# Kernel tuning notes

Hardware: AMD Instinct MI355X
Metric: run time of the kernel (lower is better)

## Reference

```python
import jax, jax.numpy as jnp
import numpy as np

L = 10
DIL = tuple(2 ** i for i in range(L))  # dilations 1..512, kernel_size=2 -> one past tap, mem_size = dilation
DMAX = max(DIL)
R = 64            # residual channels
G = 2 * R         # gate channels (tanh | sigmoid)
S = 256           # skip channels
MEL = 80
NCLS = 256
HOP = 64
END = 256
FRAMES = 8


def setup_inputs() -> dict:
    ks = jax.random.split(jax.random.key(0), 16)
    sc = jnp.float32(0.1)
    n = lambda k, shape: jax.random.normal(k, shape, jnp.float32) * sc
    return {
        "y": jax.random.normal(ks[0], (MEL, FRAMES), jnp.float32),
        "samples": jax.random.uniform(ks[1], (FRAMES * HOP,), jnp.float32),
        "c": 1,
        "emb": jnp.tanh(n(ks[2], (NCLS, R))),               # buffer already tanh'ed in __init__
        "condition_W": n(ks[3], (L * G, MEL)),
        "WV_past_weight": n(ks[4], (L, G, R, 1)),            # kernel_size=2 -> 1 past tap
        "WV_present_weight": n(ks[5], (L, G, R)),
        "W_o_weight": n(ks[6], (L - 1, R + S, R)),
        "W_o_bias": n(ks[7], (L - 1, R + S)),
        "W_o_weight_last": n(ks[8], (S, R)),
        "W_o_bias_last": n(ks[9], (S,)),
        "end1_w": n(ks[10], (END, S)),
        "end1_b": n(ks[11], (END,)),
        "end2_w": n(ks[12], (NCLS, END)),
        "end2_b": n(ks[13], (NCLS,)),
    }


def _forward(y, samples, c, emb, condition_W, WV_past, WV_pres, W_o_w, W_o_b,
             W_o_wl, W_o_bl, e1w, e1b, e2w, e2b):
    # nearest-neighbor upsample of conditioning by hop_length (F.interpolate default mode)
    y_up = jnp.repeat(y, HOP, axis=1)                        # [MEL, T]
    T = y_up.shape[1]
    conds = (condition_W @ y_up).T.reshape(T, L, G)          # precompute all conditioning projections
    dil = jnp.array(DIL, jnp.int32)
    lidx = jnp.arange(L)

    def step(carry, xs):
        hist, prev = carry                                   # hist: [L, R, DMAX] shared ring buffer, global write ptr t%DMAX
        t, cond_t, s = xs
        x = emb[prev]                                        # [R]
        # value written dil[j] steps ago (zeros before warm-up), read before this step's write
        past = hist[lidx, :, (t - dil) % DMAX]               # [L, R]
        skip = jnp.zeros((S,), hist.dtype)
        written = []
        for j in range(L):
            h = cond_t[j] + WV_past[j, :, :, 0] @ past[j] + WV_pres[j] @ x
            zw, zf = jnp.split(h, 2)
            z = jnp.tanh(zw) * jax.nn.sigmoid(zf)
            written.append(x)                                # layer j stores its input in its ring buffer
            if j < L - 1:
                o = W_o_w[j] @ z + W_o_b[j]
                x = x + o[:R]
                skip = skip + o[R:]
            else:
                skip = skip + W_o_wl @ z + W_o_bl
        hist = hist.at[:, :, t % DMAX].set(jnp.stack(written))
        hid = jax.nn.relu(e1w @ jax.nn.relu(skip) + e1b)
        logits = (e2w @ hid + e2b) * c
        # inverse-CDF sampling: first index where cumsum(softmax) exceeds the uniform sample
        new = jnp.argmax(jnp.cumsum(jax.nn.softmax(logits)) > s).astype(jnp.int32)
        return (hist, new), (new, logits)

    carry0 = (jnp.zeros((L, R, DMAX), jnp.float32), jnp.int32(NCLS // 2 - 1))
    _, (outs, logits) = jax.lax.scan(step, carry0, (jnp.arange(T), conds, samples))
    return outs, logits


def reference(y, samples, c, emb, condition_W, WV_past_weight, WV_present_weight,
              W_o_weight, W_o_bias, W_o_weight_last, W_o_bias_last,
              end1_w, end1_b, end2_w, end2_b):
    outs, _ = _forward(y, samples, c, emb, condition_W, WV_past_weight,
                       WV_present_weight, W_o_weight, W_o_bias,
                       W_o_weight_last, W_o_bias_last, end1_w, end1_b, end2_w, end2_b)
    return outs
```

## Files before the change

### kernel.cpp

```cpp
#include <hip/hip_runtime.h>
#include <cmath>

#define L_     10
#define R_     64
#define G_     128
#define S_     256
#define MEL_   80
#define NCLS_  256
#define HOP_   64
#define END_   256
#define FRAMES_ 8
#define T_     512

typedef unsigned long long u64;

#define COND8_OFF   0
#define HIST_OFF    10240
#define MBX64_OFF   (HIST_OFF + 8*T_*R_)
#define CTR64_OFF   (MBX64_OFF + 4*R_*2)
#define HID64_OFF   (CTR64_OFF + 10*S_*2)
#define FLAG_OFF    (HID64_OFF + S_*2)

#define FID_PREV   11
#define FID_CLAIM  12

#define NROLE 7
#define SPIN_CAP (1 << 16)

__device__ __forceinline__ void push_tag(u64* p, float v, int tag) {
  u64 pk = ((u64)(unsigned)tag << 32) | (unsigned)__float_as_int(v);
  __hip_atomic_store(p, pk, __ATOMIC_RELAXED, __HIP_MEMORY_SCOPE_AGENT);
}
__device__ __forceinline__ u64 atomic_slot(u64* p) {
  u64 r;
  asm volatile("global_atomic_add_x2 %0, %1, %2, off sc0\n\ts_waitcnt vmcnt(0)"
               : "=&v"(r) : "v"(p), "v"(0ULL) : "memory");
  return r;
}
__device__ __forceinline__ float poll_tag(u64* p, int want) {
  u64 r; int n = 0;
  for (;;) {
    r = ((n & 15) == 15)
            ? atomic_slot(p)
            : __hip_atomic_load(p, __ATOMIC_RELAXED, __HIP_MEMORY_SCOPE_AGENT);
    if ((int)(r >> 32) >= want) break;
    if (++n > SPIN_CAP) break;
  }
  return __int_as_float((int)(unsigned)(r & 0xffffffffULL));
}
__device__ __forceinline__ float2 poll_tag2(u64* p0, u64* p1, int want) {
  u64 r0, r1; int n = 0;
  for (;;) {
    if ((n & 15) == 15) {
      r0 = atomic_slot(p0);
      r1 = atomic_slot(p1);
    } else {
      r0 = __hip_atomic_load(p0, __ATOMIC_RELAXED, __HIP_MEMORY_SCOPE_AGENT);
      r1 = __hip_atomic_load(p1, __ATOMIC_RELAXED, __HIP_MEMORY_SCOPE_AGENT);
    }
    if ((int)(r0 >> 32) >= want && (int)(r1 >> 32) >= want) break;
    if (++n > SPIN_CAP) break;
  }
  return make_float2(__int_as_float((int)(unsigned)(r0 & 0xffffffffULL)),
                     __int_as_float((int)(unsigned)(r1 & 0xffffffffULL)));
}
__device__ __forceinline__ int flag_atomic(int* p) {
  int v;
  asm volatile("global_atomic_add %0, %1, %2, off sc0\n\ts_waitcnt vmcnt(0)"
               : "=&v"(v) : "v"(p), "v"(0) : "memory");
  return v;
}
__device__ __forceinline__ void push_flag(int* p, int v) {
  __hip_atomic_store(p, v, __ATOMIC_RELAXED, __HIP_MEMORY_SCOPE_AGENT);
}
__device__ __forceinline__ int wait_prev_wave(int* p, int want, int lane) {
  int v = 0, n = 0;
  do {
    if (lane == 0)
      v = ((n & 15) == 15)
              ? flag_atomic(p)
              : __hip_atomic_load(p, __ATOMIC_RELAXED, __HIP_MEMORY_SCOPE_AGENT);
    v = __shfl(v, 0, 64);
    if ((v >> 16) >= want) break;
  } while (++n <= SPIN_CAP);
  return v & 0xffff;
}

#define DOTREG(N4, W, V4, ACC) do { \
  _Pragma("unroll") \
  for (int k_ = 0; k_ < (N4); ++k_) { float4 a_ = (V4)[k_]; \
    ACC = fmaf((W)[4*k_+0], a_.x, ACC); ACC = fmaf((W)[4*k_+1], a_.y, ACC); \
    ACC = fmaf((W)[4*k_+2], a_.z, ACC); ACC = fmaf((W)[4*k_+3], a_.w, ACC); } \
} while (0)

#define DOTREG_RELU(N4, W, V4, ACC) do { \
  _Pragma("unroll") \
  for (int k_ = 0; k_ < (N4); ++k_) { float4 a_ = (V4)[k_]; \
    a_.x = fmaxf(a_.x, 0.f); a_.y = fmaxf(a_.y, 0.f); \
    a_.z = fmaxf(a_.z, 0.f); a_.w = fmaxf(a_.w, 0.f); \
    ACC = fmaf((W)[4*k_+0], a_.x, ACC); ACC = fmaf((W)[4*k_+1], a_.y, ACC); \
    ACC = fmaf((W)[4*k_+2], a_.z, ACC); ACC = fmaf((W)[4*k_+3], a_.w, ACC); } \
} while (0)

__global__ void cond_prep_kernel(const float* __restrict__ condW,
                                 const float* __restrict__ y,
                                 float* __restrict__ cond8) {
  int idx = blockIdx.x * blockDim.x + threadIdx.x;
  if (idx >= FRAMES_ * L_ * G_) return;
  int f = idx / (L_ * G_);
  int row = idx - f * (L_ * G_);
  float acc = 0.f;
  for (int m = 0; m < MEL_; ++m)
    acc = fmaf(condW[row * MEL_ + m], y[m * FRAMES_ + f], acc);
  cond8[f * (L_ * G_) + row] = acc;
}

__global__ __launch_bounds__(256, 1) void wavenet_pipe(
    const float* __restrict__ samples,
    const int*   __restrict__ c_ptr,
    const float* __restrict__ emb,
    const float* __restrict__ WVp,
    const float* __restrict__ WVx,
    const float* __restrict__ Wo,
    const float* __restrict__ Wob,
    const float* __restrict__ Wol,
    const float* __restrict__ Wobl,
    const float* __restrict__ e1w,
    const float* __restrict__ e1b,
    const float* __restrict__ e2w,
    const float* __restrict__ e2b,
    float* __restrict__ ws,
    int*   __restrict__ out) {

  const int tid = threadIdx.x;

  float* cond8   = ws + COND8_OFF;
  float* hist    = ws + HIST_OFF;
  u64*   mbx     = (u64*)(ws + MBX64_OFF);
  u64*   contrib = (u64*)(ws + CTR64_OFF);
  u64*   mbhid   = (u64*)(ws + HID64_OFF);
  int*   flags   = (int*)(ws + FLAG_OFF);
  int*   fprev   = flags + FID_PREV * 16;

  __shared__ __align__(16) float x_s[R_];
  __shared__ __align__(16) float xb_s[R_];
  __shared__ __align__(16) float z_s[R_];
  __shared__ __align__(16) float zb_s[R_];
  __shared__ __align__(16) float cond_a_s[FRAMES_ * G_];
  __shared__ __align__(16) float cond_b_s[FRAMES_ * G_];
  __shared__ __align__(16) float biasC_s[10 * S_];
  __shared__ __align__(16) float vec_s[S_];
  __shared__ __align__(16) float emb_s[NCLS_ * R_];
  __shared__ float wred[4], wsum[4];
  __shared__ int wcand[4];
  __shared__ int role_s;

  {
    unsigned xcc;
    asm volatile("s_getreg_b32 %0, hwreg(HW_REG_XCC_ID)" : "=s"(xcc));
    if (tid == 0) {
      int r = -1;
      if (xcc == 0) {
        int c0 = atomicAdd(flags + FID_CLAIM * 16, 1);
        if (c0 < NROLE) r = c0;
      }
      role_s = r;
    }
    __syncthreads();
  }
  const int bid = role_s;
  if (bid < 0) return;

  if (bid < 5) {
    const int k = bid;
    const int j_a = 2 * k, j_b = 2 * k + 1;
    const int dil_a = 1 << j_a, dil_b = 1 << j_b;
    const int gr = tid >> 1, gh = tid & 1;

    float wxa_w[32], wxa_f[32], wxb_w[32], wxb_f[32];
    float woa0[64], wob0[64], wex[64];
    float ba0, bb0;
    if (tid < 128) {
      const float4* p;
      p = (const float4*)(WVx + ((size_t)(j_a * G_ + gr)) * R_ + gh * 32);
      #pragma unroll
      for (int i = 0; i < 8; ++i) ((float4*)wxa_w)[i] = p[i];
      p = (const float4*)(WVx + ((size_t)(j_a * G_ + gr + 64)) * R_ + gh * 32);
      #pragma unroll
      for (int i = 0; i < 8; ++i) ((float4*)wxa_f)[i] = p[i];
      p = (const float4*)(WVx + ((size_t)(j_b * G_ + gr)) * R_ + gh * 32);
      #pragma unroll
      for (int i = 0; i < 8; ++i) ((float4*)wxb_w)[i] = p[i];
      p = (const float4*)(WVx + ((size_t)(j_b * G_ + gr + 64)) * R_ + gh * 32);
      #pragma unroll
      for (int i = 0; i < 8; ++i) ((float4*)wxb_f)[i] = p[i];
    }
    {
      const float* q = Wo + ((size_t)(j_a * (R_ + S_) + tid)) * R_;
      #pragma unroll
      for (int i = 0; i < 64; ++i) woa0[i] = q[i];
      ba0 = Wob[j_a * (R_ + S_) + tid];
      if (k < 4) {
        q = Wo + ((size_t)(j_b * (R_ + S_) + tid)) * R_;
        #pragma unroll
        for (int i = 0; i < 64; ++i) wob0[i] = q[i];
        bb0 = Wob[j_b * (R_ + S_) + tid];
      } else {
        q = Wol + (size_t)tid * R_;
        #pragma unroll
        for (int i = 0; i < 64; ++i) wob0[i] = q[i];
        bb0 = 0.f;
      }
      if (tid < 64) {
        q = Wo + ((size_t)(j_a * (R_ + S_) + 256 + tid)) * R_;
        #pragma unroll
        for (int i = 0; i < 64; ++i) wex[i] = q[i];
      } else if (tid < 128 && k < 4) {
        q = Wo + ((size_t)(j_b * (R_ + S_) + 256 + (tid - 64))) * R_;
        #pragma unroll
        for (int i = 0; i < 64; ++i) wex[i] = q[i];
      }
    }
    for (int i = tid; i < FRAMES_ * G_; i += 256) {
      cond_a_s[i] = cond8[(i >> 7) * (L_ * G_) + j_a * G_ + (i & 127)];
      cond_b_s[i] = cond8[(i >> 7) * (L_ * G_) + j_b * G_ + (i & 127)];
    }
    if (k == 0) {
      for (int i = tid; i < NCLS_ * R_ / 4; i += 256)
        ((float4*)emb_s)[i] = ((const float4*)emb)[i];
    }
    __syncthreads();
    float pd_aw = 0.f, pd_af = 0.f, pd_bw = 0.f, pd_bf = 0.f;
    if (tid < 128 && gh == 0) {
      pd_aw = cond_a_s[gr]; pd_af = cond_a_s[gr + 64];
      pd_bw = cond_b_s[gr]; pd_bf = cond_b_s[gr + 64];
    }

    float* hist_a = (k > 0) ? (hist + (size_t)(j_a - 1) * T_ * R_) : nullptr;
    float* hist_b = (k < 4) ? (hist + (size_t)(j_b - 1) * T_ * R_) : nullptr;
    u64* mbx_in    = mbx + (size_t)(k - 1) * R_;
    u64* mbx_out   = mbx + (size_t)k * R_;
    u64* contrib_a = contrib + (size_t)j_a * S_;
    u64* contrib_b = contrib + (size_t)j_b * S_;

    for (int t = 0; t < T_; ++t) {
      if (tid < 64) {
        if (k == 0) {
          int prev = 127;
          if (t > 0) prev = wait_prev_wave(fprev, t, tid);
          if (tid < 16)
            ((float4*)x_s)[tid] = ((const float4*)(emb_s + (size_t)prev * R_))[tid];
        } else {
          x_s[tid] = poll_tag(mbx_in + tid, t + 1);
        }
      }
      __syncthreads();

      if (tid < 128) {
        const float4* xs4 = (const float4*)(x_s + gh * 32);
        float vw = 0.f, vf = 0.f;
        DOTREG(8, wxa_w, xs4, vw);
        DOTREG(8, wxa_f, xs4, vf);
        vw += __shfl_down(vw, 1, 2);
        vf += __shfl_down(vf, 1, 2);
        if (gh == 0) {
          float hw = vw + pd_aw, hf = vf + pd_af;
          z_s[gr] = tanhf(hw) * (1.f / (1.f + expf(-hf)));
        }
      }
      if (hist_a && tid >= 240)
        ((float4*)(hist_a + (size_t)t * R_))[tid - 240] = ((const float4*)x_s)[tid - 240];
      __syncthreads();

      float va_keep = 0.f;
      {
        const float4* z4 = (const float4*)z_s;
        if (tid < 64) {
          float v0 = 0.f, v1 = 0.f;
          DOTREG(16, woa0, z4, v0);
          DOTREG(16, wex, z4, v1);
          xb_s[tid] = x_s[tid] + v0 + ba0;
          va_keep = v1;
        } else {
          float v0 = 0.f;
          DOTREG(16, woa0, z4, v0);
          va_keep = v0;
        }
      }
      __syncthreads();

      if (tid < 128) {
        const float4* xs4 = (const float4*)(xb_s + gh * 32);
        float vw = 0.f, vf = 0.f;
        DOTREG(8, wxb_w, xs4, vw);
        DOTREG(8, wxb_f, xs4, vf);
        vw += __shfl_down(vw, 1, 2);
        vf += __shfl_down(vf, 1, 2);
        if (gh == 0) {
          float hw = vw + pd_bw, hf = vf + pd_bf;
          zb_s[gr] = tanhf(hw) * (1.f / (1.f + expf(-hf)));
        }
      }
      if (hist_b && tid >= 240)
        ((float4*)(hist_b + (size_t)t * R_))[tid - 240] = ((const float4*)xb_s)[tid - 240];
      __syncthreads();

      {
        const float4* zb4 = (const float4*)zb_s;
        float v0 = 0.f;
        DOTREG(16, wob0, zb4, v0);
        if (k < 4) {
          if (tid < 64) {
            push_tag(mbx_out + tid, xb_s[tid] + v0 + bb0, t + 1);
            push_tag(contrib_a + 192 + tid, va_keep, t + 1);
          } else if (tid < 128) {
            float v1 = 0.f;
            DOTREG(16, wex, zb4, v1);
            push_tag(contrib_a + (tid - 64), va_keep, t + 1);
            push_tag(contrib_b + (tid - 64), v0, t + 1);
            push_tag(contrib_b + 192 + (tid - 64), v1, t + 1);
          } else {
            push_tag(contrib_a + (tid - 64), va_keep, t + 1);
            push_tag(contrib_b + (tid - 64), v0, t + 1);
          }
        } else {
          if (tid < 64) {
            push_tag(contrib_b + tid, v0, t + 1);
            push_tag(contrib_a + 192 + tid, va_keep, t + 1);
          } else {
            push_tag(contrib_a + (tid - 64), va_keep, t + 1);
            push_tag(contrib_b + tid, v0, t + 1);
          }
        }
      }

      const int tn = t + 1;
      if (tn < T_ && tid < 128) {
        const int f1 = tn >> 6;
        float wpw[32], wpf[32], pa[32];
        {
          const float4* pw = (const float4*)(WVp + ((size_t)(j_a * G_ + gr)) * R_ + gh * 32);
          const float4* pf = (const float4*)(WVp + ((size_t)(j_a * G_ + gr + 64)) * R_ + gh * 32);
          #pragma unroll
          for (int i = 0; i < 8; ++i) { ((float4*)wpw)[i] = pw[i]; ((float4*)wpf)[i] = pf[i]; }
          if (k == 0) {
            #pragma unroll
            for (int i = 0; i < 8; ++i) ((float4*)pa)[i] = ((const float4*)(x_s + gh * 32))[i];
          } else {
            const int tp = tn - dil_a;
            if (tp >= 0) {
              const float4* hp = (const float4*)(hist_a + (size_t)tp * R_ + gh * 32);
              #pragma unroll
              for (int i = 0; i < 8; ++i) ((float4*)pa)[i] = hp[i];
            } else {
              #pragma unroll
              for (int i = 0; i < 32; ++i) pa[i] = 0.f;
            }
          }
          float vw = 0.f, vf = 0.f;
          const float4* pa4 = (const float4*)pa;
          DOTREG(8, wpw, pa4, vw);
          DOTREG(8, wpf, pa4, vf);
          vw += __shfl_down(vw, 1, 2);
          vf += __shfl_down(vf, 1, 2);
          if (gh == 0) {
            pd_aw = vw + cond_a_s[f1 * G_ + gr];
            pd_af = vf + cond_a_s[f1 * G_ + gr + 64];
          }
        }
        if (k < 4) {
          const float4* pw = (const float4*)(WVp + ((size_t)(j_b * G_ + gr)) * R_ + gh * 32);
          const float4* pf = (const float4*)(WVp + ((size_t)(j_b * G_ + gr + 64)) * R_ + gh * 32);
          #pragma unroll
          for (int i = 0; i < 8; ++i) { ((float4*)wpw)[i] = pw[i]; ((float4*)wpf)[i] = pf[i]; }
          const int tp = tn - dil_b;
          if (tp >= 0) {
            const float4* hp = (const float4*)(hist_b + (size_t)tp * R_ + gh * 32);
            #pragma unroll
            for (int i = 0; i < 8; ++i) ((float4*)pa)[i] = hp[i];
          } else {
            #pragma unroll
            for (int i = 0; i < 32; ++i) pa[i] = 0.f;
          }
          float vw = 0.f, vf = 0.f;
          const float4* pa4 = (const float4*)pa;
          DOTREG(8, wpw, pa4, vw);
          DOTREG(8, wpf, pa4, vf);
          vw += __shfl_down(vw, 1, 2);
          vf += __shfl_down(vf, 1, 2);
          if (gh == 0) {
            pd_bw = vw + cond_b_s[f1 * G_ + gr];
            pd_bf = vf + cond_b_s[f1 * G_ + gr + 64];
          }
        } else {
          if (gh == 0) {
            pd_bw = cond_b_s[f1 * G_ + gr];
            pd_bf = cond_b_s[f1 * G_ + gr + 64];
          }
        }
      }
      __syncthreads();
    }

  } else if (bid == 5) {
    const int o_loc = tid >> 1, halfc = tid & 1;
    float w0[128], w1[128];
    {
      const float* p = e1w + ((size_t)o_loc) * S_ + halfc * 128;
      #pragma unroll
      for (int i = 0; i < 128; ++i) w0[i] = p[i];
      p = e1w + ((size_t)(128 + o_loc)) * S_ + halfc * 128;
      #pragma unroll
      for (int i = 0; i < 128; ++i) w1[i] = p[i];
    }
    const float bias0 = e1b[o_loc], bias1 = e1b[128 + o_loc];
    for (int i = tid; i < 10 * S_; i += 256) {
      int j = i >> 8, s = i & 255;
      biasC_s[i] = (j < 9) ? Wob[j * (R_ + S_) + 64 + s] : Wobl[s];
    }
    __syncthreads();

    for (int t = 0; t < T_; ++t) {
      float sacc = 0.f;
      for (int kk = 0; kk < 5; ++kk) {
        float2 v = poll_tag2(contrib + (size_t)(2 * kk) * S_ + tid,
                             contrib + (size_t)(2 * kk + 1) * S_ + tid, t + 1);
        sacc = (sacc + v.x) + biasC_s[(2 * kk) * S_ + tid];
        sacc = (sacc + v.y) + biasC_s[(2 * kk + 1) * S_ + tid];
      }
      vec_s[tid] = sacc;
      __syncthreads();
      const float4* s4 = (const float4*)(vec_s + halfc * 128);
      float v0 = 0.f, v1 = 0.f;
      DOTREG_RELU(32, w0, s4, v0);
      v0 += __shfl_down(v0, 1, 2);
      DOTREG_RELU(32, w1, s4, v1);
      v1 += __shfl_down(v1, 1, 2);
      if (halfc == 0) {
        push_tag(mbhid + o_loc,       fmaxf(v0 + bias0, 0.f), t + 1);
        push_tag(mbhid + 128 + o_loc, fmaxf(v1 + bias1, 0.f), t + 1);
      }
      __syncthreads();
    }

  } else {
    const int o_loc = tid >> 1, halfc = tid & 1;
    const float cf = (float)c_ptr[0];
    float w0[128], w1[128];
    {
      const float* p = e2w + ((size_t)o_loc) * END_ + halfc * 128;
      #pragma unroll
      for (int i = 0; i < 128; ++i) w0[i] = p[i];
      p = e2w + ((size_t)(128 + o_loc)) * END_ + halfc * 128;
      #pragma unroll
      for (int i = 0; i < 128; ++i) w1[i] = p[i];
    }
    const float bias0 = e2b[o_loc], bias1 = e2b[128 + o_loc];
    float* logits_s = cond_b_s;
    const int lane = tid & 63, wv = tid >> 6;

    for (int t = 0; t < T_; ++t) {
      vec_s[tid] = poll_tag(mbhid + tid, t + 1);
      __syncthreads();
      const float4* h4 = (const float4*)(vec_s + halfc * 128);
      float v0 = 0.f, v1 = 0.f;
      DOTREG(32, w0, h4, v0);
      v0 += __shfl_down(v0, 1, 2);
      DOTREG(32, w1, h4, v1);
      v1 += __shfl_down(v1, 1, 2);
      if (halfc == 0) {
        logits_s[o_loc]       = (v0 + bias0) * cf;
        logits_s[128 + o_loc] = (v1 + bias1) * cf;
      }
      __syncthreads();

      float lg = logits_s[tid];
      float m = lg;
      #pragma unroll
      for (int off = 32; off >= 1; off >>= 1) m = fmaxf(m, __shfl_xor(m, off, 64));
      if (lane == 0) wred[wv] = m;
      __syncthreads();
      m = fmaxf(fmaxf(wred[0], wred[1]), fmaxf(wred[2], wred[3]));
      float e = expf(lg - m);
      float cs = e;
      #pragma unroll
      for (int off = 1; off < 64; off <<= 1) {
        float o_ = __shfl_up(cs, off, 64);
        if (lane >= off) cs += o_;
      }
      if (lane == 63) wsum[wv] = cs;
      __syncthreads();
      float total = wsum[0] + wsum[1] + wsum[2] + wsum[3];
      float offv = 0.f;
      for (int w2 = 0; w2 < wv; ++w2) offv += wsum[w2];
      float thresh = samples[t] * total;
      bool flagb = (offv + cs) > thresh;
      unsigned long long mk = __ballot(flagb);
      if (lane == 0) wcand[wv] = mk ? (wv * 64 + __ffsll(mk) - 1) : 100000;
      __syncthreads();
      if (tid == 0) {
        int nw = min(min(wcand[0], wcand[1]), min(wcand[2], wcand[3]));
        if (nw >= 100000) nw = 0;
        out[t] = nw;
        push_flag(fprev, ((t + 1) << 16) | nw);
      }
      __syncthreads();
    }
  }
}

extern "C" void kernel_launch(void* const* d_in, const int* in_sizes, int n_in,
                              void* d_out, int out_size, void* d_ws, size_t ws_size,
                              hipStream_t stream) {
  const float* y       = (const float*)d_in[0];
  const float* samples = (const float*)d_in[1];
  const int*   c       = (const int*)d_in[2];
  const float* emb     = (const float*)d_in[3];
  const float* condW   = (const float*)d_in[4];
  const float* WVp     = (const float*)d_in[5];
  const float* WVx     = (const float*)d_in[6];
  const float* Wo      = (const float*)d_in[7];
  const float* Wob     = (const float*)d_in[8];
  const float* Wol     = (const float*)d_in[9];
  const float* Wobl    = (const float*)d_in[10];
  const float* e1w     = (const float*)d_in[11];
  const float* e1b     = (const float*)d_in[12];
  const float* e2w     = (const float*)d_in[13];
  const float* e2b     = (const float*)d_in[14];

  float* ws  = (float*)d_ws;
  int*   out = (int*)d_out;

  hipMemsetAsync((char*)d_ws + (size_t)FLAG_OFF * sizeof(float), 0,
                 16 * 16 * sizeof(int), stream);

  cond_prep_kernel<<<(FRAMES_ * L_ * G_ + 255) / 256, 256, 0, stream>>>(
      condW, y, ws + COND8_OFF);

  wavenet_pipe<<<256, 256, 0, stream>>>(samples, c, emb, WVp, WVx, Wo, Wob,
                                        Wol, Wobl, e1w, e1b, e2w, e2b, ws, out);
}
```

Measured before the change: 8.846 ms.

## Rebalance pipeline roles: two residual-chain blocks, skip projections offloaded to helper blocks

The residual chain moves from five blocks handling two layers each to two blocks handling five layers each. Fewer cross-block mailbox hand-offs sit on the per-step critical path. Skip-channel projections leave the chain blocks: layers 0-6 go to seven new helper blocks fed through z mailboxes, layers 7 and 9 to the skip-reduction block using transposed weights in LDS, and layer 8 stays on the second chain block. This shortens the serial dependency chain in exchange for more per-block register pressure, more spinning blocks, and an extra z-mailbox hop before the skip sum.

```diff
diff --git a/kernel.cpp b/kernel.cpp
--- a/kernel.cpp
+++ b/kernel.cpp
@@ -16,15 +16,16 @@
 
 #define COND8_OFF   0
 #define HIST_OFF    10240
-#define MBX64_OFF   (HIST_OFF + 8*T_*R_)
-#define CTR64_OFF   (MBX64_OFF + 4*R_*2)
+#define MBX5_OFF    (HIST_OFF + 8*T_*R_)
+#define ZMB_OFF     (MBX5_OFF + 2*R_)
+#define CTR64_OFF   (ZMB_OFF + 10*R_*2)
 #define HID64_OFF   (CTR64_OFF + 10*S_*2)
 #define FLAG_OFF    (HID64_OFF + S_*2)
 
 #define FID_PREV   11
 #define FID_CLAIM  12
 
-#define NROLE 7
+#define NROLE 11
 #define SPIN_CAP (1 << 16)
 
 __device__ __forceinline__ void push_tag(u64* p, float v, int tag) {
@@ -114,6 +115,16 @@
     acc = fmaf(condW[row * MEL_ + m], y[m * FRAMES_ + f], acc);
   cond8[f * (L_ * G_) + row] = acc;
 }
+
+#define EMB_B    0
+#define CONDW_B  65536
+#define BIASC_B  131072
+#define XBUF_B   141312
+#define ZS_B     142848
+#define Z9_B     143104
+#define VEC_B    143360
+#define LOG_B    144384
+#define POOL_SZ  145408
 
 __global__ __launch_bounds__(256, 1) void wavenet_pipe(
     const float* __restrict__ samples,
@@ -134,23 +145,26 @@
 
   const int tid = threadIdx.x;
 
-  float* cond8   = ws + COND8_OFF;
-  float* hist    = ws + HIST_OFF;
-  u64*   mbx     = (u64*)(ws + MBX64_OFF);
-  u64*   contrib = (u64*)(ws + CTR64_OFF);
-  u64*   mbhid   = (u64*)(ws + HID64_OFF);
-  int*   flags   = (int*)(ws + FLAG_OFF);
-  int*   fprev   = flags + FID_PREV * 16;
-
-  __shared__ __align__(16) float x_s[R_];
-  __shared__ __align__(16) float xb_s[R_];
-  __shared__ __align__(16) float z_s[R_];
-  __shared__ __align__(16) float zb_s[R_];
-  __shared__ __align__(16) float cond_a_s[FRAMES_ * G_];
-  __shared__ __align__(16) float cond_b_s[FRAMES_ * G_];
-  __shared__ __align__(16) float biasC_s[10 * S_];
-  __shared__ __align__(16) float vec_s[S_];
-  __shared__ __align__(16) float emb_s[NCLS_ * R_];
+  float* cond8 = ws + COND8_OFF;
+  float* hist  = ws + HIST_OFF;
+  u64*   x5mb  = (u64*)(ws + MBX5_OFF);
+  u64*   zmb   = (u64*)(ws + ZMB_OFF);
+  u64*   ctr   = (u64*)(ws + CTR64_OFF);
+  u64*   mbhid = (u64*)(ws + HID64_OFF);
+  int*   flags = (int*)(ws + FLAG_OFF);
+  int*   fprev = flags + FID_PREV * 16;
+
+  __shared__ __align__(16) char pool_s[POOL_SZ];
+  float* emb_s   = (float*)(pool_s + EMB_B);
+  float* cond5_s = (float*)(pool_s + CONDW_B);
+  float* wo7T_s  = (float*)(pool_s + EMB_B);
+  float* wolT_s  = (float*)(pool_s + CONDW_B);
+  float* biasC_s = (float*)(pool_s + BIASC_B);
+  float (*xbuf_s)[R_] = (float(*)[R_])(pool_s + XBUF_B);
+  float* z_s     = (float*)(pool_s + ZS_B);
+  float* z9_s    = (float*)(pool_s + Z9_B);
+  float* vec_s   = (float*)(pool_s + VEC_B);
+  float* logits_s= (float*)(pool_s + LOG_B);
   __shared__ float wred[4], wsum[4];
   __shared__ int wcand[4];
   __shared__ int role_s;
@@ -171,165 +185,134 @@
   const int bid = role_s;
   if (bid < 0) return;
 
-  if (bid < 5) {
-    const int k = bid;
-    const int j_a = 2 * k, j_b = 2 * k + 1;
-    const int dil_a = 1 << j_a, dil_b = 1 << j_b;
+  if (bid <= 1) {
+    const int base = (bid == 0) ? 0 : 5;
     const int gr = tid >> 1, gh = tid & 1;
 
-    float wxa_w[32], wxa_f[32], wxb_w[32], wxb_f[32];
-    float woa0[64], wob0[64], wex[64];
-    float ba0, bb0;
+    float wxw[5][32], wxf[5][32];
+    float wor[4][64], br[4];
+    float wox[64];  float bx = 0.f;
+    float wsk1[64], wsk2[64], wsk3[64];
     if (tid < 128) {
-      const float4* p;
-      p = (const float4*)(WVx + ((size_t)(j_a * G_ + gr)) * R_ + gh * 32);
-      #pragma unroll
-      for (int i = 0; i < 8; ++i) ((float4*)wxa_w)[i] = p[i];
-      p = (const float4*)(WVx + ((size_t)(j_a * G_ + gr + 64)) * R_ + gh * 32);
-      #pragma unroll
-      for (int i = 0; i < 8; ++i) ((float4*)wxa_f)[i] = p[i];
-      p = (const float4*)(WVx + ((size_t)(j_b * G_ + gr)) * R_ + gh * 32);
-      #pragma unroll
-      for (int i = 0; i < 8; ++i) ((float4*)wxb_w)[i] = p[i];
-      p = (const float4*)(WVx + ((size_t)(j_b * G_ + gr + 64)) * R_ + gh * 32);
-      #pragma unroll
-      for (int i = 0; i < 8; ++i) ((float4*)wxb_f)[i] = p[i];
-    }
-    {
-      const float* q = Wo + ((size_t)(j_a * (R_ + S_) + tid)) * R_;
-      #pragma unroll
-      for (int i = 0; i < 64; ++i) woa0[i] = q[i];
-      ba0 = Wob[j_a * (R_ + S_) + tid];
-      if (k < 4) {
-        q = Wo + ((size_t)(j_b * (R_ + S_) + tid)) * R_;
-        #pragma unroll
-        for (int i = 0; i < 64; ++i) wob0[i] = q[i];
-        bb0 = Wob[j_b * (R_ + S_) + tid];
+      #pragma unroll
+      for (int jl = 0; jl < 5; ++jl) {
+        const float4* p = (const float4*)(WVx + ((size_t)((base + jl) * G_ + gr)) * R_ + gh * 32);
+        #pragma unroll
+        for (int i = 0; i < 8; ++i) ((float4*)wxw[jl])[i] = p[i];
+        p = (const float4*)(WVx + ((size_t)((base + jl) * G_ + gr + 64)) * R_ + gh * 32);
+        #pragma unroll
+        for (int i = 0; i < 8; ++i) ((float4*)wxf[jl])[i] = p[i];
+      }
+    } else if (tid < 192) {
+      const int r = tid - 128;
+      #pragma unroll
+      for (int jl = 0; jl < 4; ++jl) {
+        const float* q = Wo + ((size_t)((base + jl) * (R_ + S_) + r)) * R_;
+        #pragma unroll
+        for (int i = 0; i < 64; ++i) wor[jl][i] = q[i];
+        br[jl] = Wob[(base + jl) * (R_ + S_) + r];
+      }
+    } else {
+      const int r = tid - 192;
+      if (bid == 0) {
+        const float* q = Wo + ((size_t)(4 * (R_ + S_) + r)) * R_;
+        #pragma unroll
+        for (int i = 0; i < 64; ++i) wox[i] = q[i];
+        bx = Wob[4 * (R_ + S_) + r];
       } else {
-        q = Wol + (size_t)tid * R_;
-        #pragma unroll
-        for (int i = 0; i < 64; ++i) wob0[i] = q[i];
-        bb0 = 0.f;
-      }
-      if (tid < 64) {
-        q = Wo + ((size_t)(j_a * (R_ + S_) + 256 + tid)) * R_;
-        #pragma unroll
-        for (int i = 0; i < 64; ++i) wex[i] = q[i];
-      } else if (tid < 128 && k < 4) {
-        q = Wo + ((size_t)(j_b * (R_ + S_) + 256 + (tid - 64))) * R_;
-        #pragma unroll
-        for (int i = 0; i < 64; ++i) wex[i] = q[i];
-      }
-    }
-    for (int i = tid; i < FRAMES_ * G_; i += 256) {
-      cond_a_s[i] = cond8[(i >> 7) * (L_ * G_) + j_a * G_ + (i & 127)];
-      cond_b_s[i] = cond8[(i >> 7) * (L_ * G_) + j_b * G_ + (i & 127)];
-    }
-    if (k == 0) {
+        const float* q = Wo + ((size_t)(8 * (R_ + S_) + 64 + 4 * r)) * R_;
+        #pragma unroll
+        for (int i = 0; i < 64; ++i) wox[i]  = q[i];
+        q += R_;
+        #pragma unroll
+        for (int i = 0; i < 64; ++i) wsk1[i] = q[i];
+        q += R_;
+        #pragma unroll
+        for (int i = 0; i < 64; ++i) wsk2[i] = q[i];
+        q += R_;
+        #pragma unroll
+        for (int i = 0; i < 64; ++i) wsk3[i] = q[i];
+      }
+    }
+    for (int jl = 0; jl < 5; ++jl)
+      for (int i = tid; i < FRAMES_ * G_; i += 256)
+        cond5_s[jl * 1024 + i] = cond8[(i >> 7) * (L_ * G_) + (base + jl) * G_ + (i & 127)];
+    if (bid == 0) {
       for (int i = tid; i < NCLS_ * R_ / 4; i += 256)
         ((float4*)emb_s)[i] = ((const float4*)emb)[i];
     }
     __syncthreads();
-    float pd_aw = 0.f, pd_af = 0.f, pd_bw = 0.f, pd_bf = 0.f;
+    float pdw[5], pdf[5];
     if (tid < 128 && gh == 0) {
-      pd_aw = cond_a_s[gr]; pd_af = cond_a_s[gr + 64];
-      pd_bw = cond_b_s[gr]; pd_bf = cond_b_s[gr + 64];
-    }
-
-    float* hist_a = (k > 0) ? (hist + (size_t)(j_a - 1) * T_ * R_) : nullptr;
-    float* hist_b = (k < 4) ? (hist + (size_t)(j_b - 1) * T_ * R_) : nullptr;
-    u64* mbx_in    = mbx + (size_t)(k - 1) * R_;
-    u64* mbx_out   = mbx + (size_t)k * R_;
-    u64* contrib_a = contrib + (size_t)j_a * S_;
-    u64* contrib_b = contrib + (size_t)j_b * S_;
+      #pragma unroll
+      for (int jl = 0; jl < 5; ++jl) {
+        pdw[jl] = cond5_s[jl * 1024 + gr];
+        pdf[jl] = cond5_s[jl * 1024 + gr + 64];
+      }
+    }
 
     for (int t = 0; t < T_; ++t) {
       if (tid < 64) {
-        if (k == 0) {
+        if (bid == 0) {
           int prev = 127;
           if (t > 0) prev = wait_prev_wave(fprev, t, tid);
           if (tid < 16)
-            ((float4*)x_s)[tid] = ((const float4*)(emb_s + (size_t)prev * R_))[tid];
+            ((float4*)xbuf_s[0])[tid] = ((const float4*)(emb_s + (size_t)prev * R_))[tid];
         } else {
-          x_s[tid] = poll_tag(mbx_in + tid, t + 1);
+          xbuf_s[0][tid] = poll_tag(x5mb + tid, t + 1);
         }
       }
       __syncthreads();
 
-      if (tid < 128) {
-        const float4* xs4 = (const float4*)(x_s + gh * 32);
-        float vw = 0.f, vf = 0.f;
-        DOTREG(8, wxa_w, xs4, vw);
-        DOTREG(8, wxa_f, xs4, vf);
-        vw += __shfl_down(vw, 1, 2);
-        vf += __shfl_down(vf, 1, 2);
-        if (gh == 0) {
-          float hw = vw + pd_aw, hf = vf + pd_af;
-          z_s[gr] = tanhf(hw) * (1.f / (1.f + expf(-hf)));
+      #pragma unroll
+      for (int jl = 0; jl < 5; ++jl) {
+        const int jg = base + jl;
+        if (tid < 128) {
+          const float4* xs4 = (const float4*)(xbuf_s[jl] + gh * 32);
+          float vw = 0.f, vf = 0.f;
+          DOTREG(8, wxw[jl], xs4, vw);
+          DOTREG(8, wxf[jl], xs4, vf);
+          vw += __shfl_down(vw, 1, 2);
+          vf += __shfl_down(vf, 1, 2);
+          if (gh == 0) {
+            float hw = vw + pdw[jl], hf = vf + pdf[jl];
+            float zv = tanhf(hw) * (1.f / (1.f + expf(-hf)));
+            z_s[gr] = zv;
+            if (jg <= 6) push_tag(zmb + jg * 64 + gr, zv, t + 1);
+            else if (jg == 7 || jg == 9) push_tag(zmb + jg * 64 + gr, zv, t + 1);
+          }
+        } else if (tid >= 192) {
+          if ((bid == 0 && jl >= 1) || (bid == 1 && jl <= 3))
+            hist[(size_t)(jg - 1) * T_ * R_ + (size_t)t * R_ + (tid - 192)] = xbuf_s[jl][tid - 192];
         }
-      }
-      if (hist_a && tid >= 240)
-        ((float4*)(hist_a + (size_t)t * R_))[tid - 240] = ((const float4*)x_s)[tid - 240];
-      __syncthreads();
-
-      float va_keep = 0.f;
-      {
-        const float4* z4 = (const float4*)z_s;
-        if (tid < 64) {
-          float v0 = 0.f, v1 = 0.f;
-          DOTREG(16, woa0, z4, v0);
-          DOTREG(16, wex, z4, v1);
-          xb_s[tid] = x_s[tid] + v0 + ba0;
-          va_keep = v1;
-        } else {
-          float v0 = 0.f;
-          DOTREG(16, woa0, z4, v0);
-          va_keep = v0;
-        }
-      }
-      __syncthreads();
-
-      if (tid < 128) {
-        const float4* xs4 = (const float4*)(xb_s + gh * 32);
-        float vw = 0.f, vf = 0.f;
-        DOTREG(8, wxb_w, xs4, vw);
-        DOTREG(8, wxb_f, xs4, vf);
-        vw += __shfl_down(vw, 1, 2);
-        vf += __shfl_down(vf, 1, 2);
-        if (gh == 0) {
-          float hw = vw + pd_bw, hf = vf + pd_bf;
-          zb_s[gr] = tanhf(hw) * (1.f / (1.f + expf(-hf)));
-        }
-      }
-      if (hist_b && tid >= 240)
-        ((float4*)(hist_b + (size_t)t * R_))[tid - 240] = ((const float4*)xb_s)[tid - 240];
-      __syncthreads();
-
-      {
-        const float4* zb4 = (const float4*)zb_s;
-        float v0 = 0.f;
-        DOTREG(16, wob0, zb4, v0);
-        if (k < 4) {
-          if (tid < 64) {
-            push_tag(mbx_out + tid, xb_s[tid] + v0 + bb0, t + 1);
-            push_tag(contrib_a + 192 + tid, va_keep, t + 1);
-          } else if (tid < 128) {
-            float v1 = 0.f;
-            DOTREG(16, wex, zb4, v1);
-            push_tag(contrib_a + (tid - 64), va_keep, t + 1);
-            push_tag(contrib_b + (tid - 64), v0, t + 1);
-            push_tag(contrib_b + 192 + (tid - 64), v1, t + 1);
-          } else {
-            push_tag(contrib_a + (tid - 64), va_keep, t + 1);
-            push_tag(contrib_b + (tid - 64), v0, t + 1);
-          }
-        } else {
-          if (tid < 64) {
-            push_tag(contrib_b + tid, v0, t + 1);
-            push_tag(contrib_a + 192 + tid, va_keep, t + 1);
-          } else {
-            push_tag(contrib_a + (tid - 64), va_keep, t + 1);
-            push_tag(contrib_b + tid, v0, t + 1);
+        __syncthreads();
+
+        if (jl < 4) {
+          if (tid >= 128 && tid < 192) {
+            const int r = tid - 128;
+            float v = 0.f;
+            DOTREG(16, wor[jl], (const float4*)z_s, v);
+            xbuf_s[jl + 1][r] = xbuf_s[jl][r] + v + br[jl];
+          }
+          if (bid == 1 && jl == 3 && tid >= 192) {
+            const int r = tid - 192;
+            float v0 = 0.f, v1 = 0.f, v2 = 0.f, v3 = 0.f;
+            DOTREG(16, wox,  (const float4*)z_s, v0);
+            DOTREG(16, wsk1, (const float4*)z_s, v1);
+            DOTREG(16, wsk2, (const float4*)z_s, v2);
+            DOTREG(16, wsk3, (const float4*)z_s, v3);
+            push_tag(ctr + 8 * 256 + 4 * r + 0, v0, t + 1);
+            push_tag(ctr + 8 * 256 + 4 * r + 1, v1, t + 1);
+            push_tag(ctr + 8 * 256 + 4 * r + 2, v2, t + 1);
+            push_tag(ctr + 8 * 256 + 4 * r + 3, v3, t + 1);
+          }
+          __syncthreads();
+        } else if (bid == 0) {
+          if (tid >= 192) {
+            const int r = tid - 192;
+            float v = 0.f;
+            DOTREG(16, wox, (const float4*)z_s, v);
+            push_tag(x5mb + r, xbuf_s[4][r] + v + bx, t + 1);
           }
         }
       }
@@ -338,18 +321,27 @@
       if (tn < T_ && tid < 128) {
         const int f1 = tn >> 6;
         float wpw[32], wpf[32], pa[32];
-        {
-          const float4* pw = (const float4*)(WVp + ((size_t)(j_a * G_ + gr)) * R_ + gh * 32);
-          const float4* pf = (const float4*)(WVp + ((size_t)(j_a * G_ + gr + 64)) * R_ + gh * 32);
+        #pragma unroll
+        for (int jl = 0; jl < 5; ++jl) {
+          const int jg = base + jl;
+          if (jg == 9) {
+            if (gh == 0) {
+              pdw[4] = cond5_s[4 * 1024 + f1 * G_ + gr];
+              pdf[4] = cond5_s[4 * 1024 + f1 * G_ + gr + 64];
+            }
+            continue;
+          }
+          const float4* pw = (const float4*)(WVp + ((size_t)(jg * G_ + gr)) * R_ + gh * 32);
+          const float4* pf = (const float4*)(WVp + ((size_t)(jg * G_ + gr + 64)) * R_ + gh * 32);
           #pragma unroll
           for (int i = 0; i < 8; ++i) { ((float4*)wpw)[i] = pw[i]; ((float4*)wpf)[i] = pf[i]; }
-          if (k == 0) {
+          if (jg == 0) {
             #pragma unroll
-            for (int i = 0; i < 8; ++i) ((float4*)pa)[i] = ((const float4*)(x_s + gh * 32))[i];
+            for (int i = 0; i < 8; ++i) ((float4*)pa)[i] = ((const float4*)(xbuf_s[0] + gh * 32))[i];
           } else {
-            const int tp = tn - dil_a;
+            const int tp = tn - (1 << jg);
             if (tp >= 0) {
-              const float4* hp = (const float4*)(hist_a + (size_t)tp * R_ + gh * 32);
+              const float4* hp = (const float4*)(hist + (size_t)(jg - 1) * T_ * R_ + (size_t)tp * R_ + gh * 32);
               #pragma unroll
               for (int i = 0; i < 8; ++i) ((float4*)pa)[i] = hp[i];
             } else {
@@ -364,45 +356,15 @@
           vw += __shfl_down(vw, 1, 2);
           vf += __shfl_down(vf, 1, 2);
           if (gh == 0) {
-            pd_aw = vw + cond_a_s[f1 * G_ + gr];
-            pd_af = vf + cond_a_s[f1 * G_ + gr + 64];
+            pdw[jl] = vw + cond5_s[jl * 1024 + f1 * G_ + gr];
+            pdf[jl] = vf + cond5_s[jl * 1024 + f1 * G_ + gr + 64];
           }
         }
-        if (k < 4) {
-          const float4* pw = (const float4*)(WVp + ((size_t)(j_b * G_ + gr)) * R_ + gh * 32);
-          const float4* pf = (const float4*)(WVp + ((size_t)(j_b * G_ + gr + 64)) * R_ + gh * 32);
-          #pragma unroll
-          for (int i = 0; i < 8; ++i) { ((float4*)wpw)[i] = pw[i]; ((float4*)wpf)[i] = pf[i]; }
-          const int tp = tn - dil_b;
-          if (tp >= 0) {
-            const float4* hp = (const float4*)(hist_b + (size_t)tp * R_ + gh * 32);
-            #pragma unroll
-            for (int i = 0; i < 8; ++i) ((float4*)pa)[i] = hp[i];
-          } else {
-            #pragma unroll
-            for (int i = 0; i < 32; ++i) pa[i] = 0.f;
-          }
-          float vw = 0.f, vf = 0.f;
-          const float4* pa4 = (const float4*)pa;
-          DOTREG(8, wpw, pa4, vw);
-          DOTREG(8, wpf, pa4, vf);
-          vw += __shfl_down(vw, 1, 2);
-          vf += __shfl_down(vf, 1, 2);
-          if (gh == 0) {
-            pd_bw = vw + cond_b_s[f1 * G_ + gr];
-            pd_bf = vf + cond_b_s[f1 * G_ + gr + 64];
-          }
-        } else {
-          if (gh == 0) {
-            pd_bw = cond_b_s[f1 * G_ + gr];
-            pd_bf = cond_b_s[f1 * G_ + gr + 64];
-          }
-        }
-      }
-      __syncthreads();
-    }
-
-  } else if (bid == 5) {
+      }
+      __syncthreads();
+    }
+
+  } else if (bid == 2) {
     const int o_loc = tid >> 1, halfc = tid & 1;
     float w0[128], w1[128];
     {
@@ -418,16 +380,35 @@
       int j = i >> 8, s = i & 255;
       biasC_s[i] = (j < 9) ? Wob[j * (R_ + S_) + 64 + s] : Wobl[s];
     }
+    for (int k = 0; k < 64; ++k) {
+      wo7T_s[k * 256 + tid] = Wo[((size_t)(7 * (R_ + S_) + 64 + tid)) * R_ + k];
+      wolT_s[k * 256 + tid] = Wol[(size_t)tid * R_ + k];
+    }
     __syncthreads();
 
     for (int t = 0; t < T_; ++t) {
+      if (tid < 64)       z_s[tid]       = poll_tag(zmb + 7 * 64 + tid, t + 1);
+      else if (tid < 128) z9_s[tid - 64] = poll_tag(zmb + 9 * 64 + (tid - 64), t + 1);
+      __syncthreads();
+      float v7 = 0.f, v9 = 0.f;
+      #pragma unroll
+      for (int k = 0; k < 64; ++k) {
+        v7 = fmaf(wo7T_s[k * 256 + tid], z_s[k],  v7);
+        v9 = fmaf(wolT_s[k * 256 + tid], z9_s[k], v9);
+      }
       float sacc = 0.f;
-      for (int kk = 0; kk < 5; ++kk) {
-        float2 v = poll_tag2(contrib + (size_t)(2 * kk) * S_ + tid,
-                             contrib + (size_t)(2 * kk + 1) * S_ + tid, t + 1);
+      for (int kk = 0; kk < 3; ++kk) {
+        float2 v = poll_tag2(ctr + (size_t)(2 * kk) * S_ + tid,
+                             ctr + (size_t)(2 * kk + 1) * S_ + tid, t + 1);
         sacc = (sacc + v.x) + biasC_s[(2 * kk) * S_ + tid];
         sacc = (sacc + v.y) + biasC_s[(2 * kk + 1) * S_ + tid];
       }
+      float v6 = poll_tag(ctr + 6 * 256 + tid, t + 1);
+      sacc = (sacc + v6) + biasC_s[6 * 256 + tid];
+      sacc = (sacc + v7) + biasC_s[7 * 256 + tid];
+      float v8 = poll_tag(ctr + 8 * 256 + tid, t + 1);
+      sacc = (sacc + v8) + biasC_s[8 * 256 + tid];
+      sacc = (sacc + v9) + biasC_s[9 * 256 + tid];
       vec_s[tid] = sacc;
       __syncthreads();
       const float4* s4 = (const float4*)(vec_s + halfc * 128);
@@ -443,7 +424,7 @@
       __syncthreads();
     }
 
-  } else {
+  } else if (bid == 3) {
     const int o_loc = tid >> 1, halfc = tid & 1;
     const float cf = (float)c_ptr[0];
     float w0[128], w1[128];
@@ -456,7 +437,6 @@
       for (int i = 0; i < 128; ++i) w1[i] = p[i];
     }
     const float bias0 = e2b[o_loc], bias1 = e2b[128 + o_loc];
-    float* logits_s = cond_b_s;
     const int lane = tid & 63, wv = tid >> 6;
 
     for (int t = 0; t < T_; ++t) {
@@ -504,6 +484,25 @@
         out[t] = nw;
         push_flag(fprev, ((t + 1) << 16) | nw);
       }
+      __syncthreads();
+    }
+
+  } else {
+    const int j = bid - 4;
+    float wsk[64];
+    {
+      const float* q = Wo + ((size_t)(j * (R_ + S_) + 64 + tid)) * R_;
+      #pragma unroll
+      for (int i = 0; i < 64; ++i) wsk[i] = q[i];
+    }
+    u64* zin  = zmb + j * 64;
+    u64* cout = ctr + (size_t)j * 256;
+    for (int t = 0; t < T_; ++t) {
+      if (tid < 64) z_s[tid] = poll_tag(zin + tid, t + 1);
+      __syncthreads();
+      float v = 0.f;
+      DOTREG(16, wsk, (const float4*)z_s, v);
+      push_tag(cout + tid, v, t + 1);
       __syncthreads();
     }
   }
```

Result: slower. 21.41 ms (+142.0%).
